# Performance work log

Hardware: AMD Instinct MI355X
Metric: run time of the kernel (lower is better)

The kernel has to match this reference:

```python
import jax, jax.numpy as jnp
import numpy as np

N, C, H, M = 4096, 1024, 16, 4096
D = C // H
EPS = 1e-6


def rms_norm(x, g):
    # RMSNorm32: normalize in fp32 with eps=1e-6, affine scale g
    x32 = x.astype(jnp.float32)
    inv = jax.lax.rsqrt(jnp.mean(x32 * x32, axis=-1, keepdims=True) + EPS)
    return (x32 * inv).astype(x.dtype) * g


def setup_inputs() -> dict:
    key = jax.random.key(0)
    ks = jax.random.split(key, 6)
    s = 1.0 / np.sqrt(C)
    return {
        "x": jax.random.normal(ks[0], (N, C), jnp.float32),
        "g1": jnp.ones((C,), jnp.float32),
        "g2": jnp.ones((C,), jnp.float32),
        "w_qkv": jax.random.normal(ks[1], (C, 3 * C), jnp.float32) * s,
        "w_o": jax.random.normal(ks[2], (C, C), jnp.float32) * s,
        "w1": jax.random.normal(ks[3], (C, M), jnp.float32) * s,
        "w2": jax.random.normal(ks[4], (M, C), jnp.float32) * (1.0 / np.sqrt(M)),
    }


def reference(x, g1, g2, w_qkv, w_o, w1, w2):
    # --- pre-norm + full multi-head self-attention over all N sparse tokens ---
    h = rms_norm(x, g1)                                   # [N, C]
    qkv = (h @ w_qkv).reshape(N, 3, H, D)                 # [N, 3, H, D]
    q, k, v = qkv[:, 0], qkv[:, 1], qkv[:, 2]             # [N, H, D]
    scale = 1.0 / np.sqrt(D)
    scores = jnp.einsum('nhd,mhd->hnm', q, k) * scale     # [H, N, N]
    attn = jax.nn.softmax(scores, axis=-1)
    o = jnp.einsum('hnm,mhd->nhd', attn, v).reshape(N, C) # [N, C]
    x = x + o @ w_o                                       # residual
    # --- pre-norm + gated-free MLP (GELU tanh) ---
    h2 = rms_norm(x, g2)
    m = jax.nn.gelu(h2 @ w1, approximate=True) @ w2       # [N, C]
    return x + m
```

## Files before the change

kernel.cpp:

```cpp
#include <hip/hip_runtime.h>
#include <stdint.h>

#define TOK 4096
#define CH  1024
#define NH  16
#define HD  64
#define FF  4096

typedef __attribute__((ext_vector_type(8))) short bf16x8;
typedef __attribute__((ext_vector_type(4))) float f32x4;
typedef __attribute__((ext_vector_type(16))) float f32x16;

__device__ __forceinline__ unsigned short f2bf(float f) {
    union { float f; unsigned u; } v; v.f = f;
    unsigned u = v.u;
    u += 0x7fffu + ((u >> 16) & 1u);
    return (unsigned short)(u >> 16);
}

__device__ __forceinline__ unsigned cvtpk(float a, float b) {
    unsigned r;
    asm("v_cvt_pk_bf16_f32 %0, %1, %2" : "=v"(r) : "v"(a), "v"(b));
    return r;
}

__device__ __forceinline__ void load_lds16(const void* g, void* l) {
    __builtin_amdgcn_global_load_lds(
        (const __attribute__((address_space(1))) unsigned int*)g,
        (__attribute__((address_space(3))) unsigned int*)l, 16, 0, 0);
}

template<int N> __device__ __forceinline__ void wait_vm_lgkm0() {
    if constexpr (N == 0)      asm volatile("s_waitcnt vmcnt(0) lgkmcnt(0)" ::: "memory");
    else if constexpr (N == 4) asm volatile("s_waitcnt vmcnt(4) lgkmcnt(0)" ::: "memory");
    else if constexpr (N == 8) asm volatile("s_waitcnt vmcnt(8) lgkmcnt(0)" ::: "memory");
    __builtin_amdgcn_sched_barrier(0);
    __builtin_amdgcn_s_barrier();
}

__device__ __forceinline__ float gelu_tanh(float u) {
    float z = 0.7978845608028654f * (u + 0.044715f * u * u * u);
    float e = __expf(2.0f * z);
    return 0.5f * u * (1.0f + (1.0f - 2.0f / (e + 1.0f)));
}

__global__ __launch_bounds__(256) void wT_kernel(const float* __restrict__ in,
                                                 unsigned short* __restrict__ out,
                                                 int K, int Nn) {
    __shared__ float tile[32][36];
    int k0 = blockIdx.x * 32, n0 = blockIdx.y * 32;
    int t = threadIdx.x;
    int r = t >> 3, c4 = (t & 7) * 4;
    float4 v = *(const float4*)(in + (size_t)(k0 + r) * Nn + n0 + c4);
    *(float4*)&tile[r][c4] = v;
    __syncthreads();
    ushort4 o;
    o.x = f2bf(tile[c4 + 0][r]);
    o.y = f2bf(tile[c4 + 1][r]);
    o.z = f2bf(tile[c4 + 2][r]);
    o.w = f2bf(tile[c4 + 3][r]);
    *(ushort4*)(out + (size_t)(n0 + r) * K + k0 + c4) = o;
}

__global__ __launch_bounds__(256) void rms_kernel(const float* __restrict__ x,
                                                  const float* __restrict__ g,
                                                  unsigned short* __restrict__ out) {
    int row = blockIdx.x, t = threadIdx.x;
    const float4* xr = (const float4*)(x + (size_t)row * CH);
    float4 v = xr[t];
    float ss = v.x * v.x + v.y * v.y + v.z * v.z + v.w * v.w;
#pragma unroll
    for (int m = 32; m; m >>= 1) ss += __shfl_xor(ss, m, 64);
    __shared__ float wsum[4];
    if ((t & 63) == 0) wsum[t >> 6] = ss;
    __syncthreads();
    float inv = rsqrtf((wsum[0] + wsum[1] + wsum[2] + wsum[3]) * (1.0f / CH) + 1e-6f);
    float4 gv = ((const float4*)g)[t];
    ushort4 o;
    o.x = f2bf(v.x * inv * gv.x);
    o.y = f2bf(v.y * inv * gv.y);
    o.z = f2bf(v.z * inv * gv.z);
    o.w = f2bf(v.w * inv * gv.w);
    ((ushort4*)(out + (size_t)row * CH))[t] = o;
}

template<int BM, int BN, int EPI>
__global__ __launch_bounds__(256) void gemm_bt(const unsigned short* __restrict__ A,
                                               const unsigned short* __restrict__ Bt,
                                               void* __restrict__ outp,
                                               const float* __restrict__ resid,
                                               int M, int Nn, int K) {
    __shared__ __align__(16) unsigned short ldsA[2][BM * 32];
    __shared__ __align__(16) unsigned short ldsB[2][BN * 32];
    const int t = threadIdx.x, l = t & 63, w = t >> 6;
    const int nbn = Nn / BN;
    const int bid = blockIdx.x, nwg = gridDim.x, cpx = nwg >> 3;
    const int swz = (bid & 7) * cpx + (bid >> 3);
    const int bm = swz / nbn, bn = swz % nbn;
    const int wr = w >> 1, wc = w & 1;
    constexpr int MF = BM / 32, NF = BN / 32;
    const unsigned short* Ag = A + (size_t)bm * BM * K;
    const unsigned short* Bg = Bt + (size_t)bn * BN * K;

    f32x4 acc[MF][NF];
#pragma unroll
    for (int m = 0; m < MF; m++)
#pragma unroll
        for (int n = 0; n < NF; n++) acc[m][n] = {0.f, 0.f, 0.f, 0.f};

    auto stage = [&](int buf, int kt) {
#pragma unroll
        for (int p = 0; p < BM / 64; p++) {
            int c = t + 256 * p;
            load_lds16(Ag + (size_t)(c >> 2) * K + kt * 32 + (c & 3) * 8, &ldsA[buf][c * 8]);
        }
#pragma unroll
        for (int p = 0; p < BN / 64; p++) {
            int c = t + 256 * p;
            load_lds16(Bg + (size_t)(c >> 2) * K + kt * 32 + (c & 3) * 8, &ldsB[buf][c * 8]);
        }
    };

    stage(0, 0);
    __syncthreads();
    const int nkt = K >> 5;
    for (int kt = 0; kt < nkt; kt++) {
        const int buf = kt & 1;
        if (kt + 1 < nkt) stage(buf ^ 1, kt + 1);
        bf16x8 af[MF], bfr[NF];
#pragma unroll
        for (int m = 0; m < MF; m++)
            af[m] = *(const bf16x8*)&ldsA[buf][(wr * (BM / 2) + m * 16 + (l & 15)) * 32 + (l >> 4) * 8];
#pragma unroll
        for (int n = 0; n < NF; n++)
            bfr[n] = *(const bf16x8*)&ldsB[buf][(wc * (BN / 2) + n * 16 + (l & 15)) * 32 + (l >> 4) * 8];
#pragma unroll
        for (int m = 0; m < MF; m++)
#pragma unroll
            for (int n = 0; n < NF; n++)
                acc[m][n] = __builtin_amdgcn_mfma_f32_16x16x32_bf16(af[m], bfr[n], acc[m][n], 0, 0, 0);
        __syncthreads();
    }

    const int r0 = bm * BM + wr * (BM / 2), c0 = bn * BN + wc * (BN / 2);
#pragma unroll
    for (int m = 0; m < MF; m++)
#pragma unroll
        for (int n = 0; n < NF; n++)
#pragma unroll
            for (int r = 0; r < 4; r++) {
                int rr = r0 + m * 16 + (l >> 4) * 4 + r;
                int cc = c0 + n * 16 + (l & 15);
                float v = acc[m][n][r];
                if (EPI == 0) {
                    ((unsigned short*)outp)[(size_t)rr * Nn + cc] = f2bf(v);
                } else if (EPI == 1) {
                    ((unsigned short*)outp)[(size_t)rr * Nn + cc] = f2bf(gelu_tanh(v));
                } else {
                    ((float*)outp)[(size_t)rr * Nn + cc] = resid[(size_t)rr * Nn + cc] + v;
                }
            }
}

template<int EPI>
__global__ __launch_bounds__(512) void gemm256(const unsigned short* __restrict__ A,
                                               const unsigned short* __restrict__ Bt,
                                               void* __restrict__ outp,
                                               unsigned short* __restrict__ vout,
                                               int M, int Nn, int K) {
    __shared__ __align__(16) unsigned short lds[2][4][8192];
    const int t = threadIdx.x, l = t & 63, w = t >> 6;
    const int wr = w >> 2, wc = w & 3;
    const int nbn = Nn >> 8;
    const int bid = blockIdx.x, nwg = gridDim.x, cpx = nwg >> 3;
    const int swz = (bid & 7) * cpx + (bid >> 3);
    const int bm = swz / nbn, bn = swz % nbn;

    const int lbase = (((l & 15) * 64 + (l >> 4) * 16)) ^ (((l >> 3) & 1) << 5);

    int srow[2], scol[2];
#pragma unroll
    for (int L = 0; L < 2; L++) {
        int g = t + L * 512;
        int s = g >> 6;
        int wb = ((g & 63) * 16) ^ (((g >> 5) & 1) << 5);
        srow[L] = (s >> 1) * 16 + (wb >> 6);
        scol[L] = (s & 1) * 32 + ((wb & 63) >> 1);
    }

    const unsigned short* Asrc = A + (size_t)(bm * 256) * K;
    const unsigned short* Bsrc = Bt + (size_t)(bn * 256) * K;

    auto stage_half = [&](int j) {
        const int kt = j >> 2, slot = j & 3;
        const unsigned short* base = (slot < 2 ? Asrc : Bsrc) + (size_t)((slot & 1) * 128) * K;
#pragma unroll
        for (int L = 0; L < 2; L++)
            load_lds16(base + (size_t)srow[L] * K + kt * 64 + scol[L],
                       &lds[kt & 1][slot][(t + L * 512) * 8]);
    };

    f32x4 acc[8][4];
#pragma unroll
    for (int m = 0; m < 8; m++)
#pragma unroll
        for (int n = 0; n < 4; n++) acc[m][n] = {0.f, 0.f, 0.f, 0.f};

    const int nkt = K >> 6;
    stage_half(0); stage_half(1); stage_half(2); stage_half(3);

    for (int kt = 0; kt < nkt; kt++) {
        wait_vm_lgkm0<0>();
        const char* Abase = (const char*)&lds[kt & 1][wr][0];
        const char* Bbase = (const char*)&lds[kt & 1][2 + (wc >> 1)][0];
        bf16x8 bfr[4][2];
#pragma unroll
        for (int q = 0; q < 4; q++) {
            if (q == 0) {
#pragma unroll
                for (int n = 0; n < 4; n++)
#pragma unroll
                    for (int ks = 0; ks < 2; ks++)
                        bfr[n][ks] = *(const bf16x8*)(Bbase + ((((wc & 1) * 4 + n) * 2 + ks) * 1024 + lbase));
            }
            bf16x8 af[2][2];
#pragma unroll
            for (int mi = 0; mi < 2; mi++)
#pragma unroll
                for (int ks = 0; ks < 2; ks++)
                    af[mi][ks] = *(const bf16x8*)(Abase + (((q * 2 + mi) * 2 + ks) * 1024 + lbase));
            if (kt + 1 < nkt) stage_half((kt + 1) * 4 + q);
            __builtin_amdgcn_s_barrier();
            __builtin_amdgcn_s_setprio(1);
#pragma unroll
            for (int mi = 0; mi < 2; mi++)
#pragma unroll
                for (int n = 0; n < 4; n++) {
                    acc[q * 2 + mi][n] = __builtin_amdgcn_mfma_f32_16x16x32_bf16(af[mi][0], bfr[n][0], acc[q * 2 + mi][n], 0, 0, 0);
                    acc[q * 2 + mi][n] = __builtin_amdgcn_mfma_f32_16x16x32_bf16(af[mi][1], bfr[n][1], acc[q * 2 + mi][n], 0, 0, 0);
                }
            __builtin_amdgcn_s_setprio(0);
            __builtin_amdgcn_s_barrier();
        }
    }

    const int r0 = bm * 256 + wr * 128, c0 = bn * 256 + wc * 64;
    const bool vpart = (EPI == 3) && (c0 >= 2048);
#pragma unroll
    for (int m = 0; m < 8; m++)
#pragma unroll
        for (int n = 0; n < 4; n++) {
            if (vpart) {
                int cc = c0 + n * 16 + (l & 15);
                int rrb = r0 + m * 16 + (l >> 4) * 4;
                ushort4 pk;
                pk.x = f2bf(acc[m][n][0]);
                pk.y = f2bf(acc[m][n][1]);
                pk.z = f2bf(acc[m][n][2]);
                pk.w = f2bf(acc[m][n][3]);
                *(ushort4*)(vout + (size_t)(cc - 2048) * 4096 + rrb) = pk;
            } else {
#pragma unroll
                for (int r = 0; r < 4; r++) {
                    int rr = r0 + m * 16 + (l >> 4) * 4 + r;
                    int cc = c0 + n * 16 + (l & 15);
                    float v = acc[m][n][r];
                    if (EPI == 1) {
                        ((unsigned short*)outp)[(size_t)rr * Nn + cc] = f2bf(gelu_tanh(v));
                    } else {
                        float sc = (cc < 1024) ? 0.180336880f : 1.0f;
                        ((unsigned short*)outp)[(size_t)rr * Nn + cc] = f2bf(v * sc);
                    }
                }
            }
        }
}

__global__ __launch_bounds__(256) void attn_kernel(const unsigned short* __restrict__ qkv,
                                                   const unsigned short* __restrict__ vT,
                                                   unsigned short* __restrict__ o) {
    __shared__ __align__(16) unsigned short Kl[4][4096];
    __shared__ __align__(16) unsigned short Vl[4][4096];
    const int t = threadIdx.x, l = t & 63, w = t >> 6;
    const int h = blockIdx.y;
    const int qrow = blockIdx.x * 128 + w * 32 + (l & 31);

    bf16x8 qf[4];
    {
        const unsigned short* qp = qkv + (size_t)qrow * 3072 + h * 64 + ((l >> 5) * 8);
#pragma unroll
        for (int c = 0; c < 4; c++) qf[c] = *(const bf16x8*)(qp + 16 * c);
    }
    const unsigned short* kb = qkv + 1024 + h * 64;
    const unsigned short* vb = vT + (size_t)h * 64 * 4096;

    int off8[4];
#pragma unroll
    for (int c = 0; c < 4; c++)
        off8[c] = (l & 31) * 64 + ((((l >> 5) + 2 * c) ^ (l & 7)) * 8);
    int kst[2], vst[2];
#pragma unroll
    for (int p = 0; p < 2; p++) {
        int c = t + 256 * p;
        int r = c >> 3, b = c & 7;
        kst[p] = r * 3072 + ((b ^ (r & 7)) * 8);
        vst[p] = r * 4096 + ((b ^ (r & 7)) * 8);
    }

    float lrun = 0.f;
    const f32x16 z16 = {0.f, 0.f, 0.f, 0.f, 0.f, 0.f, 0.f, 0.f,
                        0.f, 0.f, 0.f, 0.f, 0.f, 0.f, 0.f, 0.f};
    f32x16 accO[2];
#pragma unroll
    for (int dt = 0; dt < 2; dt++) accO[dt] = z16;

    auto stage = [&](int tile) {
        const int buf = tile & 3;
#pragma unroll
        for (int p = 0; p < 2; p++)
            load_lds16(kb + (size_t)tile * 64 * 3072 + kst[p], &Kl[buf][(t + 256 * p) * 8]);
#pragma unroll
        for (int p = 0; p < 2; p++)
            load_lds16(vb + tile * 64 + vst[p], &Vl[buf][(t + 256 * p) * 8]);
    };

    auto compute = [&](int kt) {
        const int cur = kt & 3;
        f32x16 s[2];
        __builtin_amdgcn_s_setprio(1);
#pragma unroll
        for (int st = 0; st < 2; st++) {
            bf16x8 kf0 = *(const bf16x8*)&Kl[cur][st * 2048 + off8[0]];
            s[st] = __builtin_amdgcn_mfma_f32_32x32x16_bf16(kf0, qf[0], z16, 0, 0, 0);
#pragma unroll
            for (int c = 1; c < 4; c++) {
                bf16x8 kf = *(const bf16x8*)&Kl[cur][st * 2048 + off8[c]];
                s[st] = __builtin_amdgcn_mfma_f32_32x32x16_bf16(kf, qf[c], s[st], 0, 0, 0);
            }
        }
        __builtin_amdgcn_s_setprio(0);

        float rs = 0.f;
#pragma unroll
        for (int st = 0; st < 2; st++)
#pragma unroll
            for (int i = 0; i < 16; i++) {
                float p = __builtin_amdgcn_exp2f(s[st][i]);
                s[st][i] = p;
                rs += p;
            }
        lrun += rs;

#pragma unroll
        for (int kc = 0; kc < 4; kc++) {
            const int base = 8 * (kc & 1);
            const f32x16& S = s[kc >> 1];
            unsigned w0 = cvtpk(S[base + 0], S[base + 1]);
            unsigned w1 = cvtpk(S[base + 2], S[base + 3]);
            unsigned w2 = cvtpk(S[base + 4], S[base + 5]);
            unsigned w3 = cvtpk(S[base + 6], S[base + 7]);
            asm("v_permlane32_swap_b32 %0, %1" : "+v"(w0), "+v"(w2));
            asm("v_permlane32_swap_b32 %0, %1" : "+v"(w1), "+v"(w3));
            union { unsigned u[4]; bf16x8 v; } pf;
            pf.u[0] = w0; pf.u[1] = w1; pf.u[2] = w2; pf.u[3] = w3;
            __builtin_amdgcn_s_setprio(1);
#pragma unroll
            for (int dt = 0; dt < 2; dt++) {
                bf16x8 vf = *(const bf16x8*)&Vl[cur][dt * 2048 + off8[kc]];
                accO[dt] = __builtin_amdgcn_mfma_f32_32x32x16_bf16(vf, pf.v, accO[dt], 0, 0, 0);
            }
            __builtin_amdgcn_s_setprio(0);
        }
    };

    stage(0); stage(1);
    for (int kt = 0; kt < 64; kt += 2) {
        wait_vm_lgkm0<0>();
        if (kt + 2 < 64) { stage(kt + 2); stage(kt + 3); }
        compute(kt);
        compute(kt + 1);
    }

    lrun += __shfl_xor(lrun, 32, 64);
    float inv = 1.0f / lrun;
    unsigned short* ob = o + (size_t)qrow * CH + h * 64 + 4 * (l >> 5);
#pragma unroll
    for (int dt = 0; dt < 2; dt++)
#pragma unroll
        for (int qd = 0; qd < 4; qd++) {
            ushort4 pk;
            pk.x = f2bf(accO[dt][qd * 4 + 0] * inv);
            pk.y = f2bf(accO[dt][qd * 4 + 1] * inv);
            pk.z = f2bf(accO[dt][qd * 4 + 2] * inv);
            pk.w = f2bf(accO[dt][qd * 4 + 3] * inv);
            *(ushort4*)(ob + dt * 32 + qd * 8) = pk;
        }
}

extern "C" void kernel_launch(void* const* d_in, const int* in_sizes, int n_in,
                              void* d_out, int out_size, void* d_ws, size_t ws_size,
                              hipStream_t stream) {
    const float* x     = (const float*)d_in[0];
    const float* g1    = (const float*)d_in[1];
    const float* g2    = (const float*)d_in[2];
    const float* w_qkv = (const float*)d_in[3];
    const float* w_o   = (const float*)d_in[4];
    const float* w1    = (const float*)d_in[5];
    const float* w2    = (const float*)d_in[6];

    char* ws = (char*)d_ws;
    unsigned short* wqkvT = (unsigned short*)(ws);
    unsigned short* woT   = (unsigned short*)(ws + 6291456);
    unsigned short* w1T   = (unsigned short*)(ws + 8388608);
    unsigned short* w2T   = (unsigned short*)(ws + 16777216);
    unsigned short* hbuf  = (unsigned short*)(ws + 25165824);
    unsigned short* qkv   = (unsigned short*)(ws + 33554432);
    unsigned short* obuf  = (unsigned short*)(ws + 58720256);
    float*          x2    = (float*)(ws + 67108864);
    unsigned short* abuf  = (unsigned short*)(ws + 83886080);
    unsigned short* vTb   = (unsigned short*)(ws + 83886080);

    dim3 b256(256), b512(512);
    wT_kernel<<<dim3(CH / 32, 3 * CH / 32), b256, 0, stream>>>(w_qkv, wqkvT, CH, 3 * CH);
    wT_kernel<<<dim3(CH / 32, CH / 32),     b256, 0, stream>>>(w_o,   woT,   CH, CH);
    wT_kernel<<<dim3(CH / 32, FF / 32),     b256, 0, stream>>>(w1,    w1T,   CH, FF);
    wT_kernel<<<dim3(FF / 32, CH / 32),     b256, 0, stream>>>(w2,    w2T,   FF, CH);

    rms_kernel<<<TOK, b256, 0, stream>>>(x, g1, hbuf);
    gemm256<3><<<(TOK / 256) * (3 * CH / 256), b512, 0, stream>>>(hbuf, wqkvT, qkv, vTb, TOK, 3 * CH, CH);
    attn_kernel<<<dim3(TOK / 128, NH), b256, 0, stream>>>(qkv, vTb, obuf);
    gemm_bt<64, 64, 2><<<(TOK / 64) * (CH / 64), b256, 0, stream>>>(obuf, woT, x2, x, TOK, CH, CH);
    rms_kernel<<<TOK, b256, 0, stream>>>(x2, g2, hbuf);
    gemm256<1><<<(TOK / 256) * (FF / 256), b512, 0, stream>>>(hbuf, w1T, abuf, nullptr, TOK, FF, CH);
    gemm_bt<64, 64, 2><<<(TOK / 64) * (CH / 64), b256, 0, stream>>>(abuf, w2T, (float*)d_out, x2, TOK, CH, FF);
}
```

Baseline: 286.8 us.

## Split attention over key range with combine kernel; deepen gemm_bt pipeline

```diff
diff --git a/kernel.cpp b/kernel.cpp
--- a/kernel.cpp
+++ b/kernel.cpp
@@ -16,6 +16,11 @@
     unsigned u = v.u;
     u += 0x7fffu + ((u >> 16) & 1u);
     return (unsigned short)(u >> 16);
+}
+
+__device__ __forceinline__ float bf2f(unsigned short s) {
+    union { unsigned u; float f; } v; v.u = ((unsigned)s) << 16;
+    return v.f;
 }
 
 __device__ __forceinline__ unsigned cvtpk(float a, float b) {
@@ -90,8 +95,8 @@
                                                void* __restrict__ outp,
                                                const float* __restrict__ resid,
                                                int M, int Nn, int K) {
-    __shared__ __align__(16) unsigned short ldsA[2][BM * 32];
-    __shared__ __align__(16) unsigned short ldsB[2][BN * 32];
+    __shared__ __align__(16) unsigned short ldsA[4][BM * 32];
+    __shared__ __align__(16) unsigned short ldsB[4][BN * 32];
     const int t = threadIdx.x, l = t & 63, w = t >> 6;
     const int nbn = Nn / BN;
     const int bid = blockIdx.x, nwg = gridDim.x, cpx = nwg >> 3;
@@ -108,7 +113,8 @@
 #pragma unroll
         for (int n = 0; n < NF; n++) acc[m][n] = {0.f, 0.f, 0.f, 0.f};
 
-    auto stage = [&](int buf, int kt) {
+    auto stage = [&](int kt) {
+        const int buf = kt & 3;
 #pragma unroll
         for (int p = 0; p < BM / 64; p++) {
             int c = t + 256 * p;
@@ -121,12 +127,8 @@
         }
     };
 
-    stage(0, 0);
-    __syncthreads();
-    const int nkt = K >> 5;
-    for (int kt = 0; kt < nkt; kt++) {
-        const int buf = kt & 1;
-        if (kt + 1 < nkt) stage(buf ^ 1, kt + 1);
+    auto compute = [&](int kt) {
+        const int buf = kt & 3;
         bf16x8 af[MF], bfr[NF];
 #pragma unroll
         for (int m = 0; m < MF; m++)
@@ -139,7 +141,15 @@
 #pragma unroll
             for (int n = 0; n < NF; n++)
                 acc[m][n] = __builtin_amdgcn_mfma_f32_16x16x32_bf16(af[m], bfr[n], acc[m][n], 0, 0, 0);
-        __syncthreads();
+    };
+
+    const int nkt = K >> 5;
+    stage(0); stage(1);
+    for (int kt = 0; kt < nkt; kt += 2) {
+        wait_vm_lgkm0<0>();
+        if (kt + 2 < nkt) { stage(kt + 2); stage(kt + 3); }
+        compute(kt);
+        compute(kt + 1);
     }
 
     const int r0 = bm * BM + wr * (BM / 2), c0 = bn * BN + wc * (BN / 2);
@@ -276,14 +286,17 @@
         }
 }
 
-__global__ __launch_bounds__(256) void attn_kernel(const unsigned short* __restrict__ qkv,
+__global__ __launch_bounds__(256) void attn_kernel(const unsigned short* qkv,
                                                    const unsigned short* __restrict__ vT,
-                                                   unsigned short* __restrict__ o) {
-    __shared__ __align__(16) unsigned short Kl[4][4096];
-    __shared__ __align__(16) unsigned short Vl[4][4096];
+                                                   unsigned short* p0,
+                                                   unsigned short* __restrict__ p1,
+                                                   float* __restrict__ Lbuf) {
+    __shared__ __align__(16) unsigned short Kl[2][4096];
+    __shared__ __align__(16) unsigned short Vl[2][4096];
     const int t = threadIdx.x, l = t & 63, w = t >> 6;
-    const int h = blockIdx.y;
+    const int h = blockIdx.y, z = blockIdx.z;
     const int qrow = blockIdx.x * 128 + w * 32 + (l & 31);
+    const int kt0 = z * 32;
 
     bf16x8 qf[4];
     {
@@ -314,18 +327,22 @@
 #pragma unroll
     for (int dt = 0; dt < 2; dt++) accO[dt] = z16;
 
-    auto stage = [&](int tile) {
-        const int buf = tile & 3;
+    auto stage = [&](int buf, int kt) {
 #pragma unroll
         for (int p = 0; p < 2; p++)
-            load_lds16(kb + (size_t)tile * 64 * 3072 + kst[p], &Kl[buf][(t + 256 * p) * 8]);
+            load_lds16(kb + (size_t)kt * 64 * 3072 + kst[p], &Kl[buf][(t + 256 * p) * 8]);
 #pragma unroll
         for (int p = 0; p < 2; p++)
-            load_lds16(vb + tile * 64 + vst[p], &Vl[buf][(t + 256 * p) * 8]);
+            load_lds16(vb + kt * 64 + vst[p], &Vl[buf][(t + 256 * p) * 8]);
     };
 
-    auto compute = [&](int kt) {
-        const int cur = kt & 3;
+    stage(0, kt0);
+    __syncthreads();
+
+    for (int i = 0; i < 32; i++) {
+        const int cur = i & 1;
+        if (i + 1 < 32) stage(cur ^ 1, kt0 + i + 1);
+
         f32x16 s[2];
         __builtin_amdgcn_s_setprio(1);
 #pragma unroll
@@ -344,9 +361,9 @@
 #pragma unroll
         for (int st = 0; st < 2; st++)
 #pragma unroll
-            for (int i = 0; i < 16; i++) {
-                float p = __builtin_amdgcn_exp2f(s[st][i]);
-                s[st][i] = p;
+            for (int i2 = 0; i2 < 16; i2++) {
+                float p = __builtin_amdgcn_exp2f(s[st][i2]);
+                s[st][i2] = p;
                 rs += p;
             }
         lrun += rs;
@@ -371,30 +388,42 @@
             }
             __builtin_amdgcn_s_setprio(0);
         }
-    };
-
-    stage(0); stage(1);
-    for (int kt = 0; kt < 64; kt += 2) {
-        wait_vm_lgkm0<0>();
-        if (kt + 2 < 64) { stage(kt + 2); stage(kt + 3); }
-        compute(kt);
-        compute(kt + 1);
-    }
-
-    lrun += __shfl_xor(lrun, 32, 64);
-    float inv = 1.0f / lrun;
-    unsigned short* ob = o + (size_t)qrow * CH + h * 64 + 4 * (l >> 5);
+        __syncthreads();
+    }
+
+    unsigned short* ob = (z == 0 ? p0 + (size_t)qrow * 3072 + 2048 : p1 + (size_t)qrow * 1024)
+                         + h * 64 + 4 * (l >> 5);
 #pragma unroll
     for (int dt = 0; dt < 2; dt++)
 #pragma unroll
         for (int qd = 0; qd < 4; qd++) {
             ushort4 pk;
-            pk.x = f2bf(accO[dt][qd * 4 + 0] * inv);
-            pk.y = f2bf(accO[dt][qd * 4 + 1] * inv);
-            pk.z = f2bf(accO[dt][qd * 4 + 2] * inv);
-            pk.w = f2bf(accO[dt][qd * 4 + 3] * inv);
+            pk.x = f2bf(accO[dt][qd * 4 + 0]);
+            pk.y = f2bf(accO[dt][qd * 4 + 1]);
+            pk.z = f2bf(accO[dt][qd * 4 + 2]);
+            pk.w = f2bf(accO[dt][qd * 4 + 3]);
             *(ushort4*)(ob + dt * 32 + qd * 8) = pk;
         }
+    lrun += __shfl_xor(lrun, 32, 64);
+    if (l < 32)
+        Lbuf[(size_t)z * NH * TOK + h * TOK + qrow] = lrun;
+}
+
+__global__ __launch_bounds__(256) void attn_combine(const unsigned short* __restrict__ qkvv,
+                                                    unsigned short* __restrict__ obuf,
+                                                    const float* __restrict__ Lbuf) {
+    const int row = blockIdx.x, t = threadIdx.x;
+    const int col = t * 4;
+    const int h = col >> 6;
+    float inv = 1.0f / (Lbuf[h * TOK + row] + Lbuf[NH * TOK + h * TOK + row]);
+    ushort4 a = *(const ushort4*)(qkvv + (size_t)row * 3072 + 2048 + col);
+    ushort4 b = *(const ushort4*)(obuf + (size_t)row * 1024 + col);
+    ushort4 o;
+    o.x = f2bf((bf2f(a.x) + bf2f(b.x)) * inv);
+    o.y = f2bf((bf2f(a.y) + bf2f(b.y)) * inv);
+    o.z = f2bf((bf2f(a.z) + bf2f(b.z)) * inv);
+    o.w = f2bf((bf2f(a.w) + bf2f(b.w)) * inv);
+    *(ushort4*)(obuf + (size_t)row * 1024 + col) = o;
 }
 
 extern "C" void kernel_launch(void* const* d_in, const int* in_sizes, int n_in,
@@ -428,7 +457,8 @@
 
     rms_kernel<<<TOK, b256, 0, stream>>>(x, g1, hbuf);
     gemm256<3><<<(TOK / 256) * (3 * CH / 256), b512, 0, stream>>>(hbuf, wqkvT, qkv, vTb, TOK, 3 * CH, CH);
-    attn_kernel<<<dim3(TOK / 128, NH), b256, 0, stream>>>(qkv, vTb, obuf);
+    attn_kernel<<<dim3(TOK / 128, NH, 2), b256, 0, stream>>>(qkv, vTb, qkv, obuf, x2);
+    attn_combine<<<TOK, b256, 0, stream>>>(qkv, obuf, x2);
     gemm_bt<64, 64, 2><<<(TOK / 64) * (CH / 64), b256, 0, stream>>>(obuf, woT, x2, x, TOK, CH, CH);
     rms_kernel<<<TOK, b256, 0, stream>>>(x2, g2, hbuf);
     gemm256<1><<<(TOK / 256) * (FF / 256), b512, 0, stream>>>(hbuf, w1T, abuf, nullptr, TOK, FF, CH);
```

New measurement: 294.0 us. 2.5% more time.
